# Optimization experiments

Hardware: AMD Instinct MI355X
Metric: run time of the kernel (lower is better)

Reference implementation:

```python
import jax, jax.numpy as jnp
import numpy as np

B, G, K, H, NC = 128, 12000, 512, 64, 100
FP = 2048
ALPHA = 0.1
STEPS = 10

def setup_inputs() -> dict:
    key = jax.random.key(0)
    ks = jax.random.split(key, 10)
    ctl = jax.random.normal(ks[0], (B, G), jnp.float32)
    # drug targets: sparse binary indicator per gene
    drug_targets = (jax.random.uniform(ks[1], (B, G)) < 0.01).astype(jnp.float32)
    cell_idx = jax.random.randint(ks[2], (B,), 0, NC, dtype=jnp.int32)
    drug_fp = jax.random.normal(ks[3], (B, FP), jnp.float32)  # unused in forward
    # gene->module membership (sparse-ish binary), ensure each module non-empty via deg clamp in model
    M = (jax.random.uniform(ks[4], (G, K)) < 0.02).astype(jnp.float32)
    # row-stochastic module adjacency for stable diffusion
    Araw = jax.random.uniform(ks[5], (K, K), jnp.float32)
    A = Araw / jnp.sum(Araw, axis=1, keepdims=True)
    W_in = jax.random.normal(ks[6], (2, H), jnp.float32) * 0.5
    b_in = jnp.zeros((H,), jnp.float32)
    cell_emb = jax.random.normal(ks[7], (NC, H), jnp.float32) * 0.02
    W_out = jax.random.normal(ks[8], (H, 1), jnp.float32) * 0.1
    b_out = jnp.zeros((1,), jnp.float32)
    return {"ctl": ctl, "drug_targets": drug_targets, "cell_idx": cell_idx,
            "drug_fp": drug_fp, "M": M, "A": A, "W_in": W_in, "b_in": b_in,
            "cell_emb": cell_emb, "W_out": W_out, "b_out": b_out}

def reference(ctl, drug_targets, cell_idx, drug_fp, M, A, W_in, b_in, cell_emb, W_out, b_out):
    # module degree (clamped) as in __init__
    mod_deg = jnp.maximum(jnp.sum(M, axis=0), 1.0)            # [K]
    x_gene = jnp.stack([ctl, drug_targets], axis=-1)          # [B,G,2]
    x_mod = jnp.einsum('gk,bgh->bkh', M, x_gene) / mod_deg[None, :, None]  # [B,K,2]
    S = jax.nn.relu(x_mod @ W_in + b_in)                      # [B,K,H]
    # 10-step personalized-PageRank-style diffusion over modules
    def step(Z, _):
        Z = (1.0 - ALPHA) * jnp.einsum('bkh,kl->blh', Z, A) + ALPHA * S
        return Z, None
    Z, _ = jax.lax.scan(step, S, None, length=STEPS)          # [B,K,H]
    h_gene = jnp.einsum('gk,bkh->bgh', M, Z)                  # [B,G,H]
    h_gene = h_gene + cell_emb[cell_idx][:, None, :]          # add cell embedding
    y = (h_gene @ W_out + b_out)[..., 0]                      # [B,G]
    return y
```

## Files before the change

kernel.cpp:

```cpp
#include <hip/hip_runtime.h>

#define B_    128
#define G_    12000
#define GP    12288
#define K_    512
#define H_    64
#define RW    32
#define NSEG  12
#define SEGG  1024
#define BKT   64

typedef __attribute__((ext_vector_type(8))) short bf16x8;
typedef __attribute__((ext_vector_type(4))) float f32x4;

__device__ __forceinline__ unsigned short f2bf(float x) {
    union { float f; unsigned u; } v; v.f = x;
    unsigned r = (v.u + 0x7FFFu + ((v.u >> 16) & 1u)) >> 16;
    return (unsigned short)r;
}
__device__ __forceinline__ float bf2f(unsigned short b) {
    union { float f; unsigned u; } v; v.u = ((unsigned)b) << 16;
    return v.f;
}

__device__ __forceinline__ void mm_body(int k0, int l0, float* __restrict__ sm,
        const float* __restrict__ Aop, const float* __restrict__ Bop,
        const float* __restrict__ Cop, const float* __restrict__ Dop,
        float alpha, float beta, float* __restrict__ O, float* __restrict__ O2) {
    float (*Xa)[68] = (float(*)[68])sm;
    float (*Xb)[36] = (float(*)[36])(sm + 2176);
    int tid = threadIdx.x;
    int kg = tid & 15, lg = tid >> 4;
    float acc[2][2] = {};
    for (int jj = 0; jj < K_; jj += 64) {
#pragma unroll
        for (int i = 0; i < 2; ++i) {
            int lin = tid + i * 256;
            int r = lin >> 4, c4 = lin & 15;
            *(float4*)&Xa[r][c4 * 4] =
                *(const float4*)&Aop[(size_t)(l0 + r) * K_ + jj + c4 * 4];
        }
#pragma unroll
        for (int i = 0; i < 2; ++i) {
            int lin = tid + i * 256;
            int r = lin >> 3, c4 = lin & 7;
            *(float4*)&Xb[r][c4 * 4] =
                *(const float4*)&Bop[(size_t)(jj + r) * K_ + k0 + c4 * 4];
        }
        __syncthreads();
#pragma unroll 8
        for (int j = 0; j < 64; ++j) {
            float xa0 = Xa[lg * 2][j], xa1 = Xa[lg * 2 + 1][j];
            float xb0 = Xb[j][kg * 2], xb1 = Xb[j][kg * 2 + 1];
            acc[0][0] = fmaf(xa0, xb0, acc[0][0]);
            acc[0][1] = fmaf(xa0, xb1, acc[0][1]);
            acc[1][0] = fmaf(xa1, xb0, acc[1][0]);
            acc[1][1] = fmaf(xa1, xb1, acc[1][1]);
        }
        __syncthreads();
    }
#pragma unroll
    for (int i = 0; i < 2; ++i) {
        size_t idx = (size_t)(l0 + lg * 2 + i) * K_ + k0 + kg * 2;
        float2 v;
        v.x = alpha * acc[i][0];
        v.y = alpha * acc[i][1];
        if (beta != 0.0f) {
            float2 cc = *(const float2*)&Cop[idx];
            v.x = fmaf(beta, cc.x, v.x);
            v.y = fmaf(beta, cc.y, v.y);
        }
        *(float2*)&O[idx] = v;
        if (O2) {
            float2 dd = *(const float2*)&Dop[idx];
            float2 w2; w2.x = v.x + dd.x; w2.y = v.y + dd.y;
            *(float2*)&O2[idx] = w2;
        }
    }
}

__global__ __launch_bounds__(256) void k_pre(
        const float* __restrict__ ctl, const float* __restrict__ dt,
        const float* __restrict__ M, const float* __restrict__ A,
        const int* __restrict__ cidx, const float* __restrict__ cemb,
        const float* __restrict__ W_out, const float* __restrict__ b_out,
        unsigned short* __restrict__ XpT, unsigned short* __restrict__ MTb,
        float* __restrict__ AT, float* __restrict__ U2,
        int* __restrict__ rcnt, int* __restrict__ rell,
        float* __restrict__ cvec) {
    __shared__ float t[32][33];
    int bid = blockIdx.x, tid = threadIdx.x;
    if (bid < 3072) {
        int p = bid / 12, chunk = bid % 12;
        int ch = p >> 7, b = p & 127;
        const float* src = (ch ? dt : ctl) + (size_t)b * G_;
        int g = chunk * 1024 + tid * 4;
        float x0 = 0.f, x1 = 0.f, x2 = 0.f, x3 = 0.f;
        if (g + 3 < G_) {
            float4 v = *(const float4*)&src[g];
            x0 = v.x; x1 = v.y; x2 = v.z; x3 = v.w;
        } else {
            if (g + 0 < G_) x0 = src[g + 0];
            if (g + 1 < G_) x1 = src[g + 1];
            if (g + 2 < G_) x2 = src[g + 2];
            if (g + 3 < G_) x3 = src[g + 3];
        }
        unsigned short h0 = f2bf(x0), h1 = f2bf(x1), h2 = f2bf(x2), h3 = f2bf(x3);
        ushort4 hv; hv.x = h0; hv.y = h1; hv.z = h2; hv.w = h3;
        *(ushort4*)&XpT[(size_t)p * GP + g] = hv;
        ushort4 lv;
        lv.x = f2bf(x0 - bf2f(h0)); lv.y = f2bf(x1 - bf2f(h1));
        lv.z = f2bf(x2 - bf2f(h2)); lv.w = f2bf(x3 - bf2f(h3));
        *(ushort4*)&XpT[(size_t)(p + 256) * GP + g] = lv;
    } else if (bid < 9216) {
        int id = bid - 3072;
        int gt = id % 384, kt = id / 384;
        int g0 = gt * 32, k0 = kt * 32;
        int tx = tid & 31, ty = tid >> 5;
#pragma unroll
        for (int j = 0; j < 4; ++j) {
            int g = g0 + ty + 8 * j;
            t[ty + 8 * j][tx] = (g < G_) ? M[(size_t)g * K_ + k0 + tx] : 0.0f;
        }
        __syncthreads();
#pragma unroll
        for (int j = 0; j < 4; ++j)
            MTb[(size_t)(k0 + ty + 8 * j) * GP + g0 + tx] = f2bf(t[tx][ty + 8 * j]);
    } else if (bid < 9472) {
        int id = bid - 9216;
        int x0 = (id & 15) * 32, y0 = (id >> 4) * 32;
        int tx = tid & 31, ty = tid >> 5;
#pragma unroll
        for (int j = 0; j < 4; ++j)
            t[ty + 8 * j][tx] = A[(size_t)(y0 + ty + 8 * j) * K_ + x0 + tx];
        __syncthreads();
#pragma unroll
        for (int j = 0; j < 4; ++j) {
            int row = x0 + ty + 8 * j, col = y0 + tx;
            float v = t[tx][ty + 8 * j];
            AT[(size_t)row * K_ + col] = v;
            U2[(size_t)row * K_ + col] = 0.09f * v + (row == col ? 0.1f : 0.0f);
        }
    } else if (bid < 12472) {
        int w = tid >> 6, lane = tid & 63;
        int g = (bid - 9472) * 4 + w;
        const float* Mp = M + (size_t)g * K_;
        int base = 0, outb = g * RW;
#pragma unroll
        for (int c0 = 0; c0 < K_; c0 += 64) {
            float v = Mp[c0 + lane];
            unsigned long long mask = __ballot(v != 0.0f);
            int before = __popcll(mask & ((1ull << lane) - 1ull));
            if (v != 0.0f) {
                int o = base + before;
                if (o < RW) rell[outb + o] = c0 + lane;
            }
            base += __popcll(mask);
        }
        if (lane == 0) rcnt[g] = (base <= RW) ? base : RW;
    } else {
        if (tid < B_) {
            int ci = cidx[tid];
            float acc = b_out[0];
#pragma unroll 8
            for (int h = 0; h < H_; ++h)
                acc = fmaf(cemb[ci * H_ + h], W_out[h], acc);
            cvec[tid] = acc;
        }
    }
}

__global__ __launch_bounds__(256) void k_gemm(
        const unsigned short* __restrict__ MTb, const unsigned short* __restrict__ XpT,
        float* __restrict__ Cp,
        const float* __restrict__ AT, const float* __restrict__ U2,
        float* __restrict__ M2, float* __restrict__ Yop) {
    __shared__ __align__(16) char smraw[36864];
    int bid = blockIdx.x, tid = threadIdx.x;
    if (bid < 192) {
        unsigned short (*Al)[72] = (unsigned short(*)[72])smraw;
        unsigned short (*Bl)[72] = (unsigned short(*)[72])(smraw + 18432);
        int tile = bid & 15, seg = bid >> 4;
        int m0 = (tile & 3) * 128, n0 = (tile >> 2) * 128;
        size_t gbase = (size_t)seg * SEGG;
        int wid = tid >> 6, lane = tid & 63;
        int wm = (wid >> 1) * 64, wn = (wid & 1) * 64;
        int r16 = lane & 15, kg8 = (lane >> 4) * 8;
        int ld_row = tid >> 3, ld_c8 = (tid & 7) * 8;
        f32x4 acc[4][4] = {};
        for (int kk = 0; kk < SEGG; kk += BKT) {
#pragma unroll
            for (int i = 0; i < 4; ++i) {
                int r = ld_row + 32 * i;
                *(uint4*)&Al[r][ld_c8] =
                    *(const uint4*)&MTb[(size_t)(m0 + r) * GP + gbase + kk + ld_c8];
                *(uint4*)&Bl[r][ld_c8] =
                    *(const uint4*)&XpT[(size_t)(n0 + r) * GP + gbase + kk + ld_c8];
            }
            __syncthreads();
#pragma unroll
            for (int ks = 0; ks < 2; ++ks) {
                bf16x8 af[4], bf[4];
#pragma unroll
                for (int mi = 0; mi < 4; ++mi)
                    af[mi] = *(const bf16x8*)&Al[wm + mi * 16 + r16][ks * 32 + kg8];
#pragma unroll
                for (int ni = 0; ni < 4; ++ni)
                    bf[ni] = *(const bf16x8*)&Bl[wn + ni * 16 + r16][ks * 32 + kg8];
#pragma unroll
                for (int mi = 0; mi < 4; ++mi)
#pragma unroll
                    for (int ni = 0; ni < 4; ++ni)
                        acc[mi][ni] = __builtin_amdgcn_mfma_f32_16x16x32_bf16(
                            af[mi], bf[ni], acc[mi][ni], 0, 0, 0);
            }
            __syncthreads();
        }
        float* C = Cp + (size_t)seg * (K_ * K_);
        int cr = (lane >> 4) * 4, cc = lane & 15;
#pragma unroll
        for (int mi = 0; mi < 4; ++mi)
#pragma unroll
            for (int ni = 0; ni < 4; ++ni) {
                size_t rb = (size_t)(m0 + wm + mi * 16 + cr) * K_
                          + (n0 + wn + ni * 16 + cc);
#pragma unroll
                for (int r = 0; r < 4; ++r)
                    C[rb + (size_t)r * K_] = acc[mi][ni][r];
            }
    } else {
        int id = bid - 192;
        mm_body((id & 15) * 32, (id >> 4) * 32, (float*)smraw,
                AT, AT, nullptr, U2, 0.81f, 0.0f, M2, Yop);
    }
}

__global__ __launch_bounds__(256) void k_red(
        const float* __restrict__ Cp, const unsigned short* __restrict__ MTb,
        const float* __restrict__ W_in, const float* __restrict__ b_in,
        const float* __restrict__ W_out, float* __restrict__ sout,
        const float* __restrict__ M2, const float* __restrict__ U2,
        float* __restrict__ M4, float* __restrict__ U4) {
    __shared__ __align__(16) float sm[4480];
    int bid = blockIdx.x, tid = threadIdx.x;
    if (bid < 256) {
        int kloc = tid >> 7, b = tid & 127;
        int k = bid * 2 + kloc;
        int cnt = 0;
        const unsigned short* mrow = MTb + (size_t)k * GP;
        for (int g = b; g < GP; g += 128) cnt += (mrow[g] != 0);
#pragma unroll
        for (int off = 32; off; off >>= 1) cnt += __shfl_down(cnt, off, 64);
        __shared__ int dsum[4];
        __shared__ float degs[2];
        int wv = tid >> 6;
        if ((tid & 63) == 0) dsum[wv] = cnt;
        __syncthreads();
        if (tid < 2) degs[tid] = (float)(dsum[tid * 2] + dsum[tid * 2 + 1]);
        __syncthreads();
        float x0 = 0.f, x1 = 0.f;
        for (int s = 0; s < NSEG; ++s) {
            const float* Cb = Cp + (size_t)s * (K_ * K_) + (size_t)k * K_;
            x0 += Cb[b]       + Cb[256 + b];
            x1 += Cb[128 + b] + Cb[384 + b];
        }
        float inv = 1.0f / fmaxf(degs[kloc], 1.0f);
        x0 *= inv; x1 *= inv;
        float s = 0.f;
#pragma unroll 8
        for (int h = 0; h < H_; ++h) {
            float v = fmaf(x0, W_in[h], fmaf(x1, W_in[H_ + h], b_in[h]));
            v = fmaxf(v, 0.f);
            s = fmaf(v, W_out[h], s);
        }
        sout[k * B_ + b] = s;
    } else {
        int id = bid - 256;
        int t = id & 255;
        if (id < 256)
            mm_body((t & 15) * 32, (t >> 4) * 32, sm, M2, M2, nullptr, nullptr,
                    1.0f, 0.0f, M4, nullptr);
        else
            mm_body((t & 15) * 32, (t >> 4) * 32, sm, M2, U2, U2, nullptr,
                    1.0f, 1.0f, U4, nullptr);
    }
}

__global__ __launch_bounds__(256) void k_p3(
        const float* __restrict__ M4, const float* __restrict__ U4,
        float* __restrict__ M8, float* __restrict__ U8,
        const float* __restrict__ Yop, const float* __restrict__ sout,
        float* __restrict__ q) {
    __shared__ __align__(16) float sm[4480];
    int bid = blockIdx.x, tid = threadIdx.x;
    if (bid < 512) {
        int t = bid & 255;
        if (bid < 256)
            mm_body((t & 15) * 32, (t >> 4) * 32, sm, M4, M4, nullptr, nullptr,
                    1.0f, 0.0f, M8, nullptr);
        else
            mm_body((t & 15) * 32, (t >> 4) * 32, sm, M4, U4, U4, nullptr,
                    1.0f, 1.0f, U8, nullptr);
    } else {
        int l = bid - 512;
        float* Wr  = sm;
        float* red = sm + 512;
        if (tid < 128)
            ((float4*)Wr)[tid] = ((const float4*)&Yop[(size_t)l * K_])[tid];
        __syncthreads();
        int b = tid & 127, seg = tid >> 7;
        int kb = seg * 256;
        float a0 = 0.f, a1 = 0.f, a2 = 0.f, a3 = 0.f;
#pragma unroll 4
        for (int kk = 0; kk < 256; kk += 4) {
            int k = kb + kk;
            a0 = fmaf(Wr[k + 0], sout[(k + 0) * B_ + b], a0);
            a1 = fmaf(Wr[k + 1], sout[(k + 1) * B_ + b], a1);
            a2 = fmaf(Wr[k + 2], sout[(k + 2) * B_ + b], a2);
            a3 = fmaf(Wr[k + 3], sout[(k + 3) * B_ + b], a3);
        }
        red[seg * 128 + b] = (a0 + a1) + (a2 + a3);
        __syncthreads();
        if (tid < 128)
            q[l * B_ + b] = red[b] + red[128 + b];
    }
}

__global__ __launch_bounds__(1024) void k_zfin(
        const float* __restrict__ M8, const float* __restrict__ U8,
        const float* __restrict__ q, const float* __restrict__ sout,
        float* __restrict__ z10) {
    __shared__ __align__(16) float Wr[4 * K_];
    __shared__ float red[8][2][128];
    int tid = threadIdx.x;
    int l0 = blockIdx.x * 2;
    if (tid < 256)
        ((float4*)Wr)[tid] = ((const float4*)&M8[(size_t)l0 * K_])[tid];
    else if (tid < 512)
        ((float4*)&Wr[2 * K_])[tid - 256] =
            ((const float4*)&U8[(size_t)l0 * K_])[tid - 256];
    __syncthreads();
    int b = tid & 127, seg = tid >> 7;
    int kb = seg * 64;
    float a0m = 0.f, a0u = 0.f, a1m = 0.f, a1u = 0.f;
#pragma unroll 8
    for (int kk = 0; kk < 64; ++kk) {
        int k = kb + kk;
        float qv = q[k * B_ + b];
        float sv = sout[k * B_ + b];
        a0m = fmaf(Wr[k], qv, a0m);
        a0u = fmaf(Wr[2 * K_ + k], sv, a0u);
        a1m = fmaf(Wr[K_ + k], qv, a1m);
        a1u = fmaf(Wr[3 * K_ + k], sv, a1u);
    }
    red[seg][0][b] = a0m + a0u;
    red[seg][1][b] = a1m + a1u;
    __syncthreads();
    if (tid < 256) {
        int row = tid >> 7, bb = tid & 127;
        float t = 0.f;
#pragma unroll
        for (int u = 0; u < 8; ++u) t += red[u][row][bb];
        z10[(l0 + row) * B_ + bb] = t;
    }
}

__global__ __launch_bounds__(256) void k_outs(const float* __restrict__ zf,
        const int* __restrict__ rcnt, const int* __restrict__ rell,
        const float* __restrict__ cvec, float* __restrict__ y) {
    __shared__ float sy[128][33];
    int g0 = blockIdx.x * 32;
    int tid = threadIdx.x;
    int gl = tid & 31, bt = tid >> 5;
    int g = g0 + gl;
    int n = rcnt[g];
    const int* rl = rell + g * RW;
    float4 a0 = {0,0,0,0}, a1 = {0,0,0,0}, a2 = {0,0,0,0}, a3 = {0,0,0,0};
    int j = 0;
    for (; j + 2 <= n; j += 2) {
        int k0 = rl[j], k1 = rl[j + 1];
        const float4* z0 = (const float4*)&zf[(size_t)k0 * B_ + bt * 16];
        const float4* z1 = (const float4*)&zf[(size_t)k1 * B_ + bt * 16];
        float4 p0 = z0[0], p1 = z0[1], p2 = z0[2], p3 = z0[3];
        float4 q0 = z1[0], q1 = z1[1], q2 = z1[2], q3 = z1[3];
        a0.x += p0.x + q0.x; a0.y += p0.y + q0.y; a0.z += p0.z + q0.z; a0.w += p0.w + q0.w;
        a1.x += p1.x + q1.x; a1.y += p1.y + q1.y; a1.z += p1.z + q1.z; a1.w += p1.w + q1.w;
        a2.x += p2.x + q2.x; a2.y += p2.y + q2.y; a2.z += p2.z + q2.z; a2.w += p2.w + q2.w;
        a3.x += p3.x + q3.x; a3.y += p3.y + q3.y; a3.z += p3.z + q3.z; a3.w += p3.w + q3.w;
    }
    if (j < n) {
        int k0 = rl[j];
        const float4* z0 = (const float4*)&zf[(size_t)k0 * B_ + bt * 16];
        float4 p0 = z0[0], p1 = z0[1], p2 = z0[2], p3 = z0[3];
        a0.x += p0.x; a0.y += p0.y; a0.z += p0.z; a0.w += p0.w;
        a1.x += p1.x; a1.y += p1.y; a1.z += p1.z; a1.w += p1.w;
        a2.x += p2.x; a2.y += p2.y; a2.z += p2.z; a2.w += p2.w;
        a3.x += p3.x; a3.y += p3.y; a3.z += p3.z; a3.w += p3.w;
    }
    int bb = bt * 16;
    sy[bb +  0][gl] = a0.x; sy[bb +  1][gl] = a0.y; sy[bb +  2][gl] = a0.z; sy[bb +  3][gl] = a0.w;
    sy[bb +  4][gl] = a1.x; sy[bb +  5][gl] = a1.y; sy[bb +  6][gl] = a1.z; sy[bb +  7][gl] = a1.w;
    sy[bb +  8][gl] = a2.x; sy[bb +  9][gl] = a2.y; sy[bb + 10][gl] = a2.z; sy[bb + 11][gl] = a2.w;
    sy[bb + 12][gl] = a3.x; sy[bb + 13][gl] = a3.y; sy[bb + 14][gl] = a3.z; sy[bb + 15][gl] = a3.w;
    __syncthreads();
    int rb = tid >> 1, half = tid & 1;
    float cv = cvec[rb];
    int cb = half * 16;
    float4 o0, o1, o2, o3;
    o0.x = sy[rb][cb + 0] + cv; o0.y = sy[rb][cb + 1] + cv; o0.z = sy[rb][cb + 2] + cv; o0.w = sy[rb][cb + 3] + cv;
    o1.x = sy[rb][cb + 4] + cv; o1.y = sy[rb][cb + 5] + cv; o1.z = sy[rb][cb + 6] + cv; o1.w = sy[rb][cb + 7] + cv;
    o2.x = sy[rb][cb + 8] + cv; o2.y = sy[rb][cb + 9] + cv; o2.z = sy[rb][cb +10] + cv; o2.w = sy[rb][cb +11] + cv;
    o3.x = sy[rb][cb +12] + cv; o3.y = sy[rb][cb +13] + cv; o3.z = sy[rb][cb +14] + cv; o3.w = sy[rb][cb +15] + cv;
    float* yp = &y[(size_t)rb * G_ + g0 + cb];
    *(float4*)&yp[0]  = o0;
    *(float4*)&yp[4]  = o1;
    *(float4*)&yp[8]  = o2;
    *(float4*)&yp[12] = o3;
}

extern "C" void kernel_launch(void* const* d_in, const int* in_sizes, int n_in,
                              void* d_out, int out_size, void* d_ws, size_t ws_size,
                              hipStream_t stream) {
    const float* ctl   = (const float*)d_in[0];
    const float* dt    = (const float*)d_in[1];
    const int*   cidx  = (const int*)d_in[2];
    const float* M     = (const float*)d_in[4];
    const float* A     = (const float*)d_in[5];
    const float* W_in  = (const float*)d_in[6];
    const float* b_in  = (const float*)d_in[7];
    const float* cemb  = (const float*)d_in[8];
    const float* W_out = (const float*)d_in[9];
    const float* b_out = (const float*)d_in[10];
    float* y = (float*)d_out;

    char* ws = (char*)d_ws;
    size_t o = 0;
    auto take = [&](size_t bytes) { char* p = ws + o; o = (o + bytes + 255) & ~(size_t)255; return p; };
    unsigned short* XpT = (unsigned short*)take((size_t)512 * GP * 2);
    unsigned short* MTb = (unsigned short*)take((size_t)K_ * GP * 2);
    float* Cp   = (float*)take((size_t)NSEG * K_ * K_ * 4);
    int*   rcnt = (int*)  take((size_t)G_ * 4);
    int*   rell = (int*)  take((size_t)G_ * RW * 4);
    float* cvec = (float*)take(B_ * 4);
    float* AT   = (float*)take((size_t)K_ * K_ * 4);
    float* U2   = (float*)take((size_t)K_ * K_ * 4);
    float* M2   = (float*)take((size_t)K_ * K_ * 4);
    float* Yop  = (float*)take((size_t)K_ * K_ * 4);
    float* M4   = (float*)take((size_t)K_ * K_ * 4);
    float* U4   = (float*)take((size_t)K_ * K_ * 4);
    float* M8   = (float*)take((size_t)K_ * K_ * 4);
    float* U8   = (float*)take((size_t)K_ * K_ * 4);
    float* sout = (float*)take((size_t)K_ * B_ * 4);
    float* q    = (float*)take((size_t)K_ * B_ * 4);
    float* z10  = (float*)take((size_t)K_ * B_ * 4);
    (void)ws_size; (void)in_sizes; (void)n_in; (void)out_size;

    k_pre<<<12473, 256, 0, stream>>>(ctl, dt, M, A, cidx, cemb, W_out, b_out,
                                     XpT, MTb, AT, U2, rcnt, rell, cvec);
    k_gemm<<<448, 256, 0, stream>>>(MTb, XpT, Cp, AT, U2, M2, Yop);
    k_red<<<768, 256, 0, stream>>>(Cp, MTb, W_in, b_in, W_out, sout,
                                   M2, U2, M4, U4);
    k_p3<<<1024, 256, 0, stream>>>(M4, U4, M8, U8, Yop, sout, q);
    k_zfin<<<K_ / 2, 1024, 0, stream>>>(M8, U8, q, sout, z10);
    k_outs<<<G_ / 32, 256, 0, stream>>>(z10, rcnt, rell, cvec, y);
}
```

Before: 118.7 us.

## Replace sparse gather output stage with dense bf16 MFMA GEMM over module matrix

The final gene projection now uses a dense bf16 MFMA GEMM of a row-major bf16 copy of M against a hi/lo bf16 split of the diffused features. This replaces the per-gene sparse neighbor lists (rcnt/rell) and the gather kernel. The bf16 copy of M is written during the existing transpose pass, so the separate pass that re-read M to build the sparse lists goes away. The module-degree count in k_red is also vectorized with 16-byte loads. The trade-off is a 12.6 MB extra bf16 write and a dense GEMM over K=512, doing far more arithmetic than the roughly 2% non-zero entries need. In exchange it removes the 32-entry-per-gene cap on the neighbor lists.

```diff
diff --git a/kernel.cpp b/kernel.cpp
--- a/kernel.cpp
+++ b/kernel.cpp
@@ -5,7 +5,6 @@
 #define GP    12288
 #define K_    512
 #define H_    64
-#define RW    32
 #define NSEG  12
 #define SEGG  1024
 #define BKT   64
@@ -85,8 +84,8 @@
         const int* __restrict__ cidx, const float* __restrict__ cemb,
         const float* __restrict__ W_out, const float* __restrict__ b_out,
         unsigned short* __restrict__ XpT, unsigned short* __restrict__ MTb,
+        unsigned short* __restrict__ Mb,
         float* __restrict__ AT, float* __restrict__ U2,
-        int* __restrict__ rcnt, int* __restrict__ rell,
         float* __restrict__ cvec) {
     __shared__ float t[32][33];
     int bid = blockIdx.x, tid = threadIdx.x;
@@ -120,7 +119,9 @@
 #pragma unroll
         for (int j = 0; j < 4; ++j) {
             int g = g0 + ty + 8 * j;
-            t[ty + 8 * j][tx] = (g < G_) ? M[(size_t)g * K_ + k0 + tx] : 0.0f;
+            float v = (g < G_) ? M[(size_t)g * K_ + k0 + tx] : 0.0f;
+            t[ty + 8 * j][tx] = v;
+            Mb[(size_t)g * K_ + k0 + tx] = f2bf(v);
         }
         __syncthreads();
 #pragma unroll
@@ -141,23 +142,6 @@
             AT[(size_t)row * K_ + col] = v;
             U2[(size_t)row * K_ + col] = 0.09f * v + (row == col ? 0.1f : 0.0f);
         }
-    } else if (bid < 12472) {
-        int w = tid >> 6, lane = tid & 63;
-        int g = (bid - 9472) * 4 + w;
-        const float* Mp = M + (size_t)g * K_;
-        int base = 0, outb = g * RW;
-#pragma unroll
-        for (int c0 = 0; c0 < K_; c0 += 64) {
-            float v = Mp[c0 + lane];
-            unsigned long long mask = __ballot(v != 0.0f);
-            int before = __popcll(mask & ((1ull << lane) - 1ull));
-            if (v != 0.0f) {
-                int o = base + before;
-                if (o < RW) rell[outb + o] = c0 + lane;
-            }
-            base += __popcll(mask);
-        }
-        if (lane == 0) rcnt[g] = (base <= RW) ? base : RW;
     } else {
         if (tid < B_) {
             int ci = cidx[tid];
@@ -248,7 +232,14 @@
         int k = bid * 2 + kloc;
         int cnt = 0;
         const unsigned short* mrow = MTb + (size_t)k * GP;
-        for (int g = b; g < GP; g += 128) cnt += (mrow[g] != 0);
+#pragma unroll
+        for (int i = 0; i < 12; ++i) {
+            uint4 v = *(const uint4*)&mrow[i * 1024 + b * 8];
+            cnt += ((v.x & 0xFFFFu) != 0) + ((v.x >> 16) != 0);
+            cnt += ((v.y & 0xFFFFu) != 0) + ((v.y >> 16) != 0);
+            cnt += ((v.z & 0xFFFFu) != 0) + ((v.z >> 16) != 0);
+            cnt += ((v.w & 0xFFFFu) != 0) + ((v.w >> 16) != 0);
+        }
 #pragma unroll
         for (int off = 32; off; off >>= 1) cnt += __shfl_down(cnt, off, 64);
         __shared__ int dsum[4];
@@ -329,7 +320,7 @@
 __global__ __launch_bounds__(1024) void k_zfin(
         const float* __restrict__ M8, const float* __restrict__ U8,
         const float* __restrict__ q, const float* __restrict__ sout,
-        float* __restrict__ z10) {
+        unsigned short* __restrict__ zbT) {
     __shared__ __align__(16) float Wr[4 * K_];
     __shared__ float red[8][2][128];
     int tid = threadIdx.x;
@@ -361,61 +352,79 @@
         float t = 0.f;
 #pragma unroll
         for (int u = 0; u < 8; ++u) t += red[u][row][bb];
-        z10[(l0 + row) * B_ + bb] = t;
-    }
-}
-
-__global__ __launch_bounds__(256) void k_outs(const float* __restrict__ zf,
-        const int* __restrict__ rcnt, const int* __restrict__ rell,
+        unsigned short hi = f2bf(t);
+        unsigned short lo = f2bf(t - bf2f(hi));
+        zbT[(size_t)bb * (2 * K_) + (l0 + row)]      = hi;
+        zbT[(size_t)bb * (2 * K_) + K_ + (l0 + row)] = lo;
+    }
+}
+
+__global__ __launch_bounds__(256) void k_yg(
+        const unsigned short* __restrict__ Mb, const unsigned short* __restrict__ zbT,
         const float* __restrict__ cvec, float* __restrict__ y) {
-    __shared__ float sy[128][33];
-    int g0 = blockIdx.x * 32;
+    __shared__ __align__(16) unsigned short Al[128][72];
+    __shared__ __align__(16) unsigned short Bh[128][72];
+    __shared__ __align__(16) unsigned short Bl2[128][72];
     int tid = threadIdx.x;
-    int gl = tid & 31, bt = tid >> 5;
-    int g = g0 + gl;
-    int n = rcnt[g];
-    const int* rl = rell + g * RW;
-    float4 a0 = {0,0,0,0}, a1 = {0,0,0,0}, a2 = {0,0,0,0}, a3 = {0,0,0,0};
-    int j = 0;
-    for (; j + 2 <= n; j += 2) {
-        int k0 = rl[j], k1 = rl[j + 1];
-        const float4* z0 = (const float4*)&zf[(size_t)k0 * B_ + bt * 16];
-        const float4* z1 = (const float4*)&zf[(size_t)k1 * B_ + bt * 16];
-        float4 p0 = z0[0], p1 = z0[1], p2 = z0[2], p3 = z0[3];
-        float4 q0 = z1[0], q1 = z1[1], q2 = z1[2], q3 = z1[3];
-        a0.x += p0.x + q0.x; a0.y += p0.y + q0.y; a0.z += p0.z + q0.z; a0.w += p0.w + q0.w;
-        a1.x += p1.x + q1.x; a1.y += p1.y + q1.y; a1.z += p1.z + q1.z; a1.w += p1.w + q1.w;
-        a2.x += p2.x + q2.x; a2.y += p2.y + q2.y; a2.z += p2.z + q2.z; a2.w += p2.w + q2.w;
-        a3.x += p3.x + q3.x; a3.y += p3.y + q3.y; a3.z += p3.z + q3.z; a3.w += p3.w + q3.w;
-    }
-    if (j < n) {
-        int k0 = rl[j];
-        const float4* z0 = (const float4*)&zf[(size_t)k0 * B_ + bt * 16];
-        float4 p0 = z0[0], p1 = z0[1], p2 = z0[2], p3 = z0[3];
-        a0.x += p0.x; a0.y += p0.y; a0.z += p0.z; a0.w += p0.w;
-        a1.x += p1.x; a1.y += p1.y; a1.z += p1.z; a1.w += p1.w;
-        a2.x += p2.x; a2.y += p2.y; a2.z += p2.z; a2.w += p2.w;
-        a3.x += p3.x; a3.y += p3.y; a3.z += p3.z; a3.w += p3.w;
-    }
-    int bb = bt * 16;
-    sy[bb +  0][gl] = a0.x; sy[bb +  1][gl] = a0.y; sy[bb +  2][gl] = a0.z; sy[bb +  3][gl] = a0.w;
-    sy[bb +  4][gl] = a1.x; sy[bb +  5][gl] = a1.y; sy[bb +  6][gl] = a1.z; sy[bb +  7][gl] = a1.w;
-    sy[bb +  8][gl] = a2.x; sy[bb +  9][gl] = a2.y; sy[bb + 10][gl] = a2.z; sy[bb + 11][gl] = a2.w;
-    sy[bb + 12][gl] = a3.x; sy[bb + 13][gl] = a3.y; sy[bb + 14][gl] = a3.z; sy[bb + 15][gl] = a3.w;
-    __syncthreads();
-    int rb = tid >> 1, half = tid & 1;
-    float cv = cvec[rb];
-    int cb = half * 16;
-    float4 o0, o1, o2, o3;
-    o0.x = sy[rb][cb + 0] + cv; o0.y = sy[rb][cb + 1] + cv; o0.z = sy[rb][cb + 2] + cv; o0.w = sy[rb][cb + 3] + cv;
-    o1.x = sy[rb][cb + 4] + cv; o1.y = sy[rb][cb + 5] + cv; o1.z = sy[rb][cb + 6] + cv; o1.w = sy[rb][cb + 7] + cv;
-    o2.x = sy[rb][cb + 8] + cv; o2.y = sy[rb][cb + 9] + cv; o2.z = sy[rb][cb +10] + cv; o2.w = sy[rb][cb +11] + cv;
-    o3.x = sy[rb][cb +12] + cv; o3.y = sy[rb][cb +13] + cv; o3.z = sy[rb][cb +14] + cv; o3.w = sy[rb][cb +15] + cv;
-    float* yp = &y[(size_t)rb * G_ + g0 + cb];
-    *(float4*)&yp[0]  = o0;
-    *(float4*)&yp[4]  = o1;
-    *(float4*)&yp[8]  = o2;
-    *(float4*)&yp[12] = o3;
+    int g0 = blockIdx.x * 128;
+    int wid = tid >> 6, lane = tid & 63;
+    int wm = (wid >> 1) * 64, wn = (wid & 1) * 64;
+    int r16 = lane & 15, kg8 = (lane >> 4) * 8;
+    int ld_row = tid >> 3, ld_c8 = (tid & 7) * 8;
+    f32x4 acc[4][4] = {};
+    for (int kk = 0; kk < K_; kk += BKT) {
+#pragma unroll
+        for (int i = 0; i < 4; ++i) {
+            int r = ld_row + 32 * i;
+            *(uint4*)&Al[r][ld_c8] =
+                *(const uint4*)&Mb[(size_t)(g0 + r) * K_ + kk + ld_c8];
+            *(uint4*)&Bh[r][ld_c8] =
+                *(const uint4*)&zbT[(size_t)r * (2 * K_) + kk + ld_c8];
+            *(uint4*)&Bl2[r][ld_c8] =
+                *(const uint4*)&zbT[(size_t)r * (2 * K_) + K_ + kk + ld_c8];
+        }
+        __syncthreads();
+#pragma unroll
+        for (int ks = 0; ks < 2; ++ks) {
+            bf16x8 af[4], bh[4], bl[4];
+#pragma unroll
+            for (int mi = 0; mi < 4; ++mi)
+                af[mi] = *(const bf16x8*)&Al[wm + mi * 16 + r16][ks * 32 + kg8];
+#pragma unroll
+            for (int ni = 0; ni < 4; ++ni) {
+                bh[ni] = *(const bf16x8*)&Bh[wn + ni * 16 + r16][ks * 32 + kg8];
+                bl[ni] = *(const bf16x8*)&Bl2[wn + ni * 16 + r16][ks * 32 + kg8];
+            }
+#pragma unroll
+            for (int mi = 0; mi < 4; ++mi)
+#pragma unroll
+                for (int ni = 0; ni < 4; ++ni) {
+                    acc[mi][ni] = __builtin_amdgcn_mfma_f32_16x16x32_bf16(
+                        af[mi], bh[ni], acc[mi][ni], 0, 0, 0);
+                    acc[mi][ni] = __builtin_amdgcn_mfma_f32_16x16x32_bf16(
+                        af[mi], bl[ni], acc[mi][ni], 0, 0, 0);
+                }
+        }
+        __syncthreads();
+    }
+    int cr = (lane >> 4) * 4, cc = lane & 15;
+#pragma unroll
+    for (int ni = 0; ni < 4; ++ni) {
+        int b = wn + ni * 16 + cc;
+        float cv = cvec[b];
+#pragma unroll
+        for (int mi = 0; mi < 4; ++mi) {
+            int g = g0 + wm + mi * 16 + cr;
+            if (g < G_) {
+                float4 o;
+                o.x = acc[mi][ni][0] + cv;
+                o.y = acc[mi][ni][1] + cv;
+                o.z = acc[mi][ni][2] + cv;
+                o.w = acc[mi][ni][3] + cv;
+                *(float4*)&y[(size_t)b * G_ + g] = o;
+            }
+        }
+    }
 }
 
 extern "C" void kernel_launch(void* const* d_in, const int* in_sizes, int n_in,
@@ -438,9 +447,9 @@
     auto take = [&](size_t bytes) { char* p = ws + o; o = (o + bytes + 255) & ~(size_t)255; return p; };
     unsigned short* XpT = (unsigned short*)take((size_t)512 * GP * 2);
     unsigned short* MTb = (unsigned short*)take((size_t)K_ * GP * 2);
+    unsigned short* Mb  = (unsigned short*)take((size_t)GP * K_ * 2);
+    unsigned short* zbT = (unsigned short*)take((size_t)B_ * 2 * K_ * 2);
     float* Cp   = (float*)take((size_t)NSEG * K_ * K_ * 4);
-    int*   rcnt = (int*)  take((size_t)G_ * 4);
-    int*   rell = (int*)  take((size_t)G_ * RW * 4);
     float* cvec = (float*)take(B_ * 4);
     float* AT   = (float*)take((size_t)K_ * K_ * 4);
     float* U2   = (float*)take((size_t)K_ * K_ * 4);
@@ -452,15 +461,14 @@
     float* U8   = (float*)take((size_t)K_ * K_ * 4);
     float* sout = (float*)take((size_t)K_ * B_ * 4);
     float* q    = (float*)take((size_t)K_ * B_ * 4);
-    float* z10  = (float*)take((size_t)K_ * B_ * 4);
     (void)ws_size; (void)in_sizes; (void)n_in; (void)out_size;
 
-    k_pre<<<12473, 256, 0, stream>>>(ctl, dt, M, A, cidx, cemb, W_out, b_out,
-                                     XpT, MTb, AT, U2, rcnt, rell, cvec);
+    k_pre<<<9473, 256, 0, stream>>>(ctl, dt, M, A, cidx, cemb, W_out, b_out,
+                                    XpT, MTb, Mb, AT, U2, cvec);
     k_gemm<<<448, 256, 0, stream>>>(MTb, XpT, Cp, AT, U2, M2, Yop);
     k_red<<<768, 256, 0, stream>>>(Cp, MTb, W_in, b_in, W_out, sout,
                                    M2, U2, M4, U4);
     k_p3<<<1024, 256, 0, stream>>>(M4, U4, M8, U8, Yop, sout, q);
-    k_zfin<<<K_ / 2, 1024, 0, stream>>>(M8, U8, q, sout, z10);
-    k_outs<<<G_ / 32, 256, 0, stream>>>(z10, rcnt, rell, cvec, y);
-}
+    k_zfin<<<K_ / 2, 1024, 0, stream>>>(M8, U8, q, sout, zbT);
+    k_yg<<<(G_ + 127) / 128, 256, 0, stream>>>(Mb, zbT, cvec, y);
+}
```

Result: faster. 110.8 us (-6.7%).
